# Performance work log

Hardware: AMD Instinct MI355X
Metric: run time of the kernel (lower is better)

## Reference

```python
import jax, jax.numpy as jnp
import numpy as np

N_NODES = 50000
N_EDGES = 500000
IN_DIM = 32
HID = 64
NUM_GRAPHS = 64


def _inv(d):
    # 1/d with inf -> 0, as in PyG HypergraphConv
    return jnp.where(d > 0, 1.0 / d, 0.0)


def hypergraph_conv(xh, row0, row1, W, b, n_hnodes, n_hedges):
    """PyG HypergraphConv (heads=1, no attention, unit hyperedge weights).
    xh: (n_hnodes, din) hyper-node features; row0: hyper-node ids, row1: hyperedge ids.
    Index n_hnodes / n_hedges is a padding slot for masked-out incidences.
    """
    xw = xh @ W                                   # (n_hnodes, dout) Theta
    xw = jnp.concatenate([xw, jnp.zeros((1, xw.shape[1]), xw.dtype)], axis=0)
    ones = jnp.ones(row0.shape[0], xw.dtype)
    D = _inv(jax.ops.segment_sum(ones, row0, num_segments=n_hnodes + 1))  # node degree^-1
    B = _inv(jax.ops.segment_sum(ones, row1, num_segments=n_hedges + 1))  # edge size^-1
    # node -> hyperedge aggregation, scaled by B
    he = jax.ops.segment_sum(xw[row0], row1, num_segments=n_hedges + 1) * B[:, None]
    # hyperedge -> node aggregation, scaled by D
    out = jax.ops.segment_sum(he[row1], row0, num_segments=n_hnodes + 1) * D[:, None]
    return out[:n_hnodes] + b


def setup_inputs() -> dict:
    key = jax.random.key(0)
    ks = jax.random.split(key, 12)
    x = jax.random.normal(ks[0], (N_NODES, 16), jnp.float32)
    edge_attr = jax.random.normal(ks[1], (N_EDGES, IN_DIM), jnp.float32)
    edge_index = jax.random.randint(ks[2], (2, N_EDGES), 0, N_NODES, dtype=jnp.int64)
    batch = jnp.sort(jax.random.randint(ks[3], (N_NODES,), 0, NUM_GRAPHS, dtype=jnp.int64))
    node_imp = jax.random.uniform(ks[4], (N_NODES,), jnp.float32)
    s = 0.05
    W0 = jax.random.normal(ks[5], (IN_DIM, HID), jnp.float32) * s
    b0 = jax.random.normal(ks[6], (HID,), jnp.float32) * s
    W1 = jax.random.normal(ks[7], (HID, HID), jnp.float32) * s
    b1 = jax.random.normal(ks[8], (HID,), jnp.float32) * s
    W2 = jax.random.normal(ks[9], (HID, HID), jnp.float32) * s
    b2 = jax.random.normal(ks[10], (HID,), jnp.float32) * s
    return {"x": x, "edge_attr": edge_attr, "edge_index": edge_index, "batch": batch,
            "node_imp": node_imp, "W0": W0, "b0": b0, "W1": W1, "b1": b1,
            "W2": W2, "b2": b2, "num_graphs": NUM_GRAPHS}


def reference(x, edge_attr, edge_index, batch, node_imp, W0, b0, W1, b1, W2, b2, num_graphs):
    N = x.shape[0]
    E = edge_index.shape[1]
    edge_imp = jnp.minimum(node_imp[edge_index[0]], node_imp[edge_index[1]])
    # --- Dual Hypergraph Transform (get_DHT) ---
    row0 = jnp.repeat(jnp.arange(E), 2)            # hyper-node = original edge id
    row1 = edge_index.T.reshape(-1)                # hyperedge  = original node id
    deg = jax.ops.segment_sum(jnp.ones(2 * E, jnp.float32), row1, num_segments=N)
    keep = deg[row1] != 1.0                        # drop incidences of degree-1 hyperedges
    row0 = jnp.where(keep, row0, E)                # redirect dropped entries to padding slot
    row1 = jnp.where(keep, row1, N + E)
    # self-loops: hyperedge ids N..N+E-1 (equivalent to torch's max_edge+1.., since
    # unused hyperedge slots receive nothing and B^-1 there is 0)
    row0 = jnp.concatenate([row0, jnp.arange(E)])
    row1 = jnp.concatenate([row1, N + jnp.arange(E)])
    edge_batch = batch[edge_index[0]]              # == hyperedge_index[1].reshape(-1,2)[:,0]
    # --- conv stack (dropout in eval mode = identity) ---
    h = edge_attr * edge_imp[:, None]
    xs = []
    for (W, b) in ((W0, b0), (W1, b1), (W2, b2)):
        h = jax.nn.relu(hypergraph_conv(h, row0, row1, W, b, E, N + E))
        h = h * edge_imp[:, None]
        xs.append(h)
    gh = jnp.concatenate(
        [jax.ops.segment_sum(h_i, edge_batch, num_segments=num_graphs) for h_i in xs], axis=1)
    return gh
```

## Files before the change

### kernel.cpp

```cpp
#include <hip/hip_runtime.h>
#include <hip/hip_bf16.h>
#include <cstdint>
#include <cstddef>

typedef unsigned short u16;
typedef unsigned int   u32;
typedef short bf16x8 __attribute__((ext_vector_type(8)));
typedef float f32x4  __attribute__((ext_vector_type(4)));

struct __align__(16) ERec { u32 uv; float iu, iv, ie; };
struct __align__(8) NRec { float dinv; float imp; };

#define NCOPY 8

__device__ __forceinline__ float bf2f(u16 v){ return __uint_as_float(((u32)v)<<16); }
__device__ __forceinline__ u16 f2bf(float f){
  u32 x = __float_as_uint(f);
  return (u16)((x + 0x7FFFu + ((x>>16)&1u)) >> 16);
}
__device__ __forceinline__ void atomAddF(float* p, float v){ unsafeAtomicAdd(p, v); }
__device__ __forceinline__ float rlanef(float v, int q){
  return __int_as_float(__builtin_amdgcn_readlane(__float_as_int(v), q));
}

__global__ void kzero(int* p, int n){
  int i = blockIdx.x*blockDim.x + threadIdx.x;
  if(i < n) p[i] = 0;
}

__global__ void kdeg2p(const int* __restrict__ ei0, const int* __restrict__ ei1,
                       int* __restrict__ deg0c, int* __restrict__ deg1c,
                       int* __restrict__ r0, int* __restrict__ r1,
                       int N, int E){
  int e = blockIdx.x*blockDim.x + threadIdx.x;
  if(e >= E) return;
  const int c = blockIdx.x & (NCOPY-1);
  r0[e] = atomicAdd(&deg0c[c*N + ei0[e]], 1);
  r1[e] = atomicAdd(&deg1c[c*N + ei1[e]], 1);
}

__global__ void kreduce(const int* __restrict__ deg0c, const int* __restrict__ deg1c,
                        int* __restrict__ deg0, int* __restrict__ deg1,
                        int* __restrict__ cb0, int* __restrict__ cb1, int N){
  int i = blockIdx.x*blockDim.x + threadIdx.x;
  if(i < N){
    int s = 0;
    #pragma unroll
    for(int c = 0; c < NCOPY; c++){ int t = deg0c[c*N+i]; cb0[c*N+i] = s; s += t; }
    deg0[i] = s;
  } else if(i < 2*N){
    int j = i - N;
    int s = 0;
    #pragma unroll
    for(int c = 0; c < NCOPY; c++){ int t = deg1c[c*N+j]; cb1[c*N+j] = s; s += t; }
    deg1[j] = s;
  }
}

__global__ __launch_bounds__(256) void ktilesum(const int* __restrict__ deg0,
                                                const int* __restrict__ deg1,
                                                int* __restrict__ tsum,
                                                int N, int nt){
  __shared__ int sh[256];
  const int b = blockIdx.x;
  const int* deg = (b < nt) ? deg0 : deg1;
  const int tile = (b < nt) ? b : b - nt;
  const int t = threadIdx.x;
  const int i = tile*256 + t;
  sh[t] = (i < N) ? deg[i] : 0;
  __syncthreads();
  for(int s = 128; s > 0; s >>= 1){
    if(t < s) sh[t] += sh[t+s];
    __syncthreads();
  }
  if(t == 0) tsum[b] = sh[0];
}
__global__ __launch_bounds__(256) void kmid(int* __restrict__ tsum,
                                            int* __restrict__ off0,
                                            int* __restrict__ off1,
                                            int N, int nt){
  __shared__ int sh[256];
  const int b = blockIdx.x;
  int* ts = tsum + b*nt;
  const int t = threadIdx.x;
  sh[t] = (t < nt) ? ts[t] : 0;
  __syncthreads();
  for(int s = 1; s < 256; s <<= 1){
    int x = (t >= s) ? sh[t-s] : 0;
    __syncthreads();
    sh[t] += x;
    __syncthreads();
  }
  if(t < nt) ts[t] = (t == 0) ? 0 : sh[t-1];
  if(t == 255){ int* off = b ? off1 : off0; off[N] = sh[255]; }
}
__global__ __launch_bounds__(256) void kapply(const int* __restrict__ deg0,
                                              const int* __restrict__ deg1,
                                              const int* __restrict__ tsum,
                                              int* __restrict__ off0,
                                              int* __restrict__ off1,
                                              const float* __restrict__ nimp,
                                              NRec* __restrict__ nrec,
                                              int N, int nt){
  __shared__ int sh[256];
  const int b = blockIdx.x;
  const int* deg = (b < nt) ? deg0 : deg1;
  int*       off = (b < nt) ? off0 : off1;
  const int tile = (b < nt) ? b : b - nt;
  const int base = tsum[b];
  const int t = threadIdx.x;
  const int i = tile*256 + t;
  sh[t] = (i < N) ? deg[i] : 0;
  __syncthreads();
  for(int s = 1; s < 256; s <<= 1){
    int x = (t >= s) ? sh[t-s] : 0;
    __syncthreads();
    sh[t] += x;
    __syncthreads();
  }
  if(i < N){
    off[i] = base + ((t == 0) ? 0 : sh[t-1]);
    if(b < nt){
      int d = deg0[i] + deg1[i];
      NRec r;
      r.dinv = (d > 1) ? (1.f/(float)d) : 0.f;
      r.imp  = nimp[i];
      nrec[i] = r;
    }
  }
}

__global__ void kpermv(const int* __restrict__ ei0, const int* __restrict__ ei1,
                       const NRec* __restrict__ nrec,
                       const int* __restrict__ off0, const int* __restrict__ off1,
                       const int* __restrict__ cb0, const int* __restrict__ cb1,
                       const int* __restrict__ r0, const int* __restrict__ r1,
                       ERec* __restrict__ rec, int* __restrict__ orig,
                       int* __restrict__ list1, int E, int N){
  int e = blockIdx.x*blockDim.x + threadIdx.x;
  if(e >= E) return;
  const int c = blockIdx.x & (NCOPY-1);
  int u = ei0[e], v = ei1[e];
  NRec ru = nrec[u];
  NRec rv = nrec[v];
  int pos = off0[u] + cb0[c*N+u] + r0[e];
  float ie = fminf(ru.imp, rv.imp);
  ERec r;
  r.uv = (u32)u | ((u32)v << 16);
  r.iu = ru.dinv; r.iv = rv.dinv; r.ie = ie;
  rec[pos]  = r;
  orig[pos] = e;
  int p1 = off1[v] + cb1[c*N+v] + r1[e];
  list1[p1] = pos;
}

__global__ __launch_bounds__(256) void kprep0(const float* __restrict__ ea,
                                              const int* __restrict__ orig,
                                              const float* __restrict__ recf,
                                              u16* __restrict__ h0, int E){
  int idx = blockIdx.x*256 + threadIdx.x;
  int row = idx >> 2;
  int c   = (idx & 3)*8;
  if(row >= E) return;
  int oe = orig[row];
  float ie = recf[(size_t)row*4 + 3];
  const float* s = ea + (size_t)oe*32 + c;
  f32x4 v0 = *(const f32x4*)s;
  f32x4 v1 = *(const f32x4*)(s+4);
  u32 o0 = (u32)f2bf(v0.x*ie) | ((u32)f2bf(v0.y*ie) << 16);
  u32 o1 = (u32)f2bf(v0.z*ie) | ((u32)f2bf(v0.w*ie) << 16);
  u32 o2 = (u32)f2bf(v1.x*ie) | ((u32)f2bf(v1.y*ie) << 16);
  u32 o3 = (u32)f2bf(v1.z*ie) | ((u32)f2bf(v1.w*ie) << 16);
  *(uint4*)(h0 + (size_t)row*32 + c) = make_uint4(o0,o1,o2,o3);
}

__global__ void kprepw(const float* __restrict__ W0, u16* __restrict__ wf0,
                       const float* __restrict__ W1, u16* __restrict__ wf1,
                       const float* __restrict__ W2, u16* __restrict__ wf2){
  const int b = blockIdx.x;
  const float* W; u16* wf; int NC, sbase;
  if(b == 0){ W = W0; wf = wf0; NC = 1; sbase = 0; }
  else if(b <= 2){ W = W1; wf = wf1; NC = 2; sbase = (b-1)*256; }
  else { W = W2; wf = wf2; NC = 2; sbase = (b-3)*256; }
  int s = sbase + threadIdx.x;
  if(s >= 4*NC*64) return;
  int lane = s & 63;
  int c    = (s >> 6) % NC;
  int tt   = s / (NC*64);
  int n  = tt*16 + (lane & 15);
  int k0 = c*32 + (lane >> 4)*8;
  #pragma unroll
  for(int j = 0; j < 8; j++)
    wf[(size_t)s*8 + j] = f2bf(W[(size_t)(k0 + j)*64 + n]);
}

template<int DIM>
__global__ __launch_bounds__(256) void kagg(const u16* __restrict__ buf,
                                            const int* __restrict__ off0,
                                            const int* __restrict__ off1,
                                            const int* __restrict__ list1,
                                            u16* __restrict__ heb, int N){
  const int t = threadIdx.x, wv = t >> 6, lane = t & 63;
  const int n = blockIdx.x*4 + wv;
  if(n >= N) return;
  constexpr int CB = DIM/8;
  constexpr int RS = 64/CB;
  const int rsub = lane / CB, cb = lane % CB;
  float acc[8];
  #pragma unroll
  for(int k = 0; k < 8; k++) acc[k] = 0.f;

  auto accum = [&](uint4 x){
    acc[0] += bf2f((u16)x.x); acc[1] += bf2f((u16)(x.x>>16));
    acc[2] += bf2f((u16)x.y); acc[3] += bf2f((u16)(x.y>>16));
    acc[4] += bf2f((u16)x.z); acc[5] += bf2f((u16)(x.z>>16));
    acc[6] += bf2f((u16)x.w); acc[7] += bf2f((u16)(x.w>>16));
  };
  const uint4 zero4 = {0,0,0,0};

  {
    const int s0 = off0[n], d0 = off0[n+1] - s0;
    const u16* base = buf + (size_t)s0*DIM;
    int j = 0;
    for(; j + RS <= d0; j += RS)
      accum(*(const uint4*)(base + (size_t)(j+rsub)*DIM + cb*8));
    if(j < d0)
      accum((rsub < d0-j) ? *(const uint4*)(base + (size_t)(j+rsub)*DIM + cb*8) : zero4);
  }
  {
    const int s1 = off1[n], d1 = off1[n+1] - s1;
    int j = 0;
    for(; j + RS <= d1; j += RS){
      int e = list1[s1 + j + rsub];
      accum(*(const uint4*)(buf + (size_t)e*DIM + cb*8));
    }
    if(j < d1){
      uint4 x = zero4;
      if(rsub < d1-j){
        int e = list1[s1 + j + rsub];
        x = *(const uint4*)(buf + (size_t)e*DIM + cb*8);
      }
      accum(x);
    }
  }
  #pragma unroll
  for(int m = CB; m <= 32; m <<= 1)
    #pragma unroll
    for(int k = 0; k < 8; k++) acc[k] += __shfl_xor(acc[k], m);
  if(rsub == 0){
    u32 o[4];
    #pragma unroll
    for(int k = 0; k < 4; k++)
      o[k] = (u32)f2bf(acc[2*k]) | ((u32)f2bf(acc[2*k+1]) << 16);
    *(uint4*)(heb + (size_t)n*DIM + cb*8) = make_uint4(o[0],o[1],o[2],o[3]);
  }
}

__global__ __launch_bounds__(256, 3) void kfusedR1(const u16* __restrict__ h0,
                                                   const u16* __restrict__ agg0,
                                                   u16* __restrict__ buf,
                                                   const f32x4* __restrict__ rec4,
                                                   const int* __restrict__ batch,
                                                   const float* __restrict__ bias0,
                                                   const u16* __restrict__ wf0,
                                                   const u16* __restrict__ wf1,
                                                   float* __restrict__ gh0,
                                                   int E){
  __shared__ __align__(16) u16 hT[4*16*72];
  __shared__ float ies[4][16];
  const int t = threadIdx.x, wv = t >> 6, lane = t & 63;
  const int quad = lane >> 4, l15 = lane & 15;
  const int c32  = lane & 31;
  const int half = lane >> 5;
  u16* hTw = &hT[wv*1152];

  float bd4[4];
  #pragma unroll
  for(int tt = 0; tt < 4; tt++) bd4[tt] = bias0[tt*16 + l15];

  bf16x8 b0fr[4];
  #pragma unroll
  for(int i = 0; i < 4; i++)
    b0fr[i] = *(const bf16x8*)(wf0 + ((size_t)i*64 + lane)*8);
  bf16x8 b1fr[8];
  #pragma unroll
  for(int i = 0; i < 8; i++)
    b1fr[i] = *(const bf16x8*)(wf1 + ((size_t)i*64 + lane)*8);

  float pool[4] = {0.f,0.f,0.f,0.f};
  int cur_g = -1;
  const int base = __builtin_amdgcn_readfirstlane((int)(blockIdx.x*256) + wv*64);

  auto flushPool = [&](){
    #pragma unroll
    for(int tt = 0; tt < 4; tt++){
      float s = pool[tt];
      s += __shfl_xor(s, 16);
      s += __shfl_xor(s, 32);
      if(quad == 0) atomAddF(&gh0[cur_g*192 + tt*16 + l15], s);
      pool[tt] = 0.f;
    }
  };

  u32 uvp = 0; f32x4 cf = {0.f,0.f,0.f,0.f}; int bt = 0;
  if(base < E){
    f32x4 w0 = rec4[(size_t)(base+l15)];
    uvp = __float_as_uint(w0.x);
    const float iu = w0.y, iv = w0.z;
    const float rc = (iu > 0.f && iv > 0.f) ? (1.f/3.f)
                   : ((iu > 0.f || iv > 0.f) ? 0.5f : 1.f);
    cf.x = rc; cf.y = iu*rc; cf.z = iv*rc; cf.w = w0.w;
    bt  = batch[uvp & 0xffffu];
  }

  #pragma unroll 1
  for(int it = 0; it < 4; it++){
    const int r0 = base + it*16;
    if(r0 < E){
      u16 zb[8], hu[8], hv[8];
      const u16* h0r = h0 + (size_t)r0*32;
      #pragma unroll
      for(int q = 0; q < 8; q++){
        const u32 uvA = (u32)__builtin_amdgcn_readlane((int)uvp, 2*q);
        const u32 uvB = (u32)__builtin_amdgcn_readlane((int)uvp, 2*q+1);
        const u32 uvS = half ? uvB : uvA;
        hv[q] = agg0[(size_t)(uvS >> 16)*32 + c32];
        hu[q] = agg0[(size_t)(uvS & 0xffffu)*32 + c32];
        zb[q] = h0r[(2*q+half)*32 + c32];
      }
      u32 uvpN = uvp; f32x4 cfN = cf; int btN = bt;
      if(it < 3){
        const int r1 = r0 + 16;
        if(r1 < E){
          f32x4 w0 = rec4[(size_t)(r1+l15)];
          uvpN = __float_as_uint(w0.x);
          const float iu = w0.y, iv = w0.z;
          const float rc = (iu > 0.f && iv > 0.f) ? (1.f/3.f)
                         : ((iu > 0.f || iv > 0.f) ? 0.5f : 1.f);
          cfN.x = rc; cfN.y = iu*rc; cfN.z = iv*rc; cfN.w = w0.w;
          btN  = batch[uvpN & 0xffffu];
        }
      }
      if(lane < 16) ies[wv][lane] = cf.w;
      #pragma unroll
      for(int q = 0; q < 8; q++){
        const float rcA = rlanef(cf.x, 2*q), rcB = rlanef(cf.x, 2*q+1);
        const float iuA = rlanef(cf.y, 2*q), iuB = rlanef(cf.y, 2*q+1);
        const float ivA = rlanef(cf.z, 2*q), ivB = rlanef(cf.z, 2*q+1);
        const float rc   = half ? rcB : rcA;
        const float iurc = half ? iuB : iuA;
        const float ivrc = half ? ivB : ivA;
        float z = fmaf(bf2f(zb[q]), rc,
                  fmaf(bf2f(hu[q]), iurc, bf2f(hv[q])*ivrc));
        hTw[(2*q+half)*72 + c32] = f2bf(z);
      }
      bf16x8 za = *(const bf16x8*)&hTw[l15*72 + quad*8];
      f32x4 a0_[4];
      #pragma unroll
      for(int tt = 0; tt < 4; tt++){
        f32x4 a = {0.f,0.f,0.f,0.f};
        a = __builtin_amdgcn_mfma_f32_16x16x32_bf16(za, b0fr[tt], a, 0, 0, 0);
        a0_[tt] = a;
      }
      float ier[4];
      #pragma unroll
      for(int r = 0; r < 4; r++) ier[r] = ies[wv][quad*4 + r];
      float o[4][4];
      #pragma unroll
      for(int tt = 0; tt < 4; tt++)
        #pragma unroll
        for(int r = 0; r < 4; r++)
          o[tt][r] = fmaxf(a0_[tt][r] + bd4[tt], 0.f) * ier[r];
      const int bFirst = __builtin_amdgcn_readlane(bt, 0);
      const int bLast  = __builtin_amdgcn_readlane(bt, 15);
      if(bFirst == bLast){
        if(bFirst != cur_g){
          if(cur_g >= 0) flushPool();
          cur_g = bFirst;
        }
        #pragma unroll
        for(int tt = 0; tt < 4; tt++)
          pool[tt] += (o[tt][0] + o[tt][1]) + (o[tt][2] + o[tt][3]);
      } else {
        #pragma unroll
        for(int rr = 0; rr < 16; rr++){
          const int bq = __builtin_amdgcn_readlane(bt, rr);
          if(bq != cur_g){
            if(cur_g >= 0) flushPool();
            cur_g = bq;
          }
          if((rr >> 2) == quad){
            #pragma unroll
            for(int tt = 0; tt < 4; tt++) pool[tt] += o[tt][rr & 3];
          }
        }
      }
      #pragma unroll
      for(int tt = 0; tt < 4; tt++)
        #pragma unroll
        for(int r = 0; r < 4; r++)
          hTw[(quad*4 + r)*72 + tt*16 + l15] = f2bf(o[tt][r]);
      bf16x8 afr0 = *(const bf16x8*)&hTw[l15*72 + quad*8];
      bf16x8 afr1 = *(const bf16x8*)&hTw[l15*72 + 32 + quad*8];
      #pragma unroll
      for(int tt = 0; tt < 4; tt++){
        f32x4 a = {0.f,0.f,0.f,0.f};
        a = __builtin_amdgcn_mfma_f32_16x16x32_bf16(afr0, b1fr[tt*2+0], a, 0, 0, 0);
        a = __builtin_amdgcn_mfma_f32_16x16x32_bf16(afr1, b1fr[tt*2+1], a, 0, 0, 0);
        const int n = tt*16 + l15;
        #pragma unroll
        for(int r = 0; r < 4; r++)
          buf[(size_t)(r0 + quad*4 + r)*64 + n] = f2bf(a[r]);
      }
      uvp = uvpN; cf = cfN; bt = btN;
    }
  }
  if(cur_g >= 0) flushPool();
}

template<bool DO_GEMM>
__global__ __launch_bounds__(256, 3) void kfused(u16* __restrict__ buf,
                                                 const u16* __restrict__ heb,
                                                 const f32x4* __restrict__ rec4,
                                                 const int* __restrict__ batch,
                                                 const float* __restrict__ bias,
                                                 const u16* __restrict__ wf,
                                                 float* __restrict__ ghL,
                                                 int E){
  constexpr int HTSZ = DO_GEMM ? 4*16*72 : 4;
  __shared__ __align__(16) u16 hT[HTSZ];
  const int t = threadIdx.x, wv = t >> 6, lane = t & 63;
  const int quad = lane >> 4, l15 = lane & 15;
  const float bd = bias[lane];

  bf16x8 bfr[8];
  if(DO_GEMM){
    #pragma unroll
    for(int i = 0; i < 8; i++)
      bfr[i] = *(const bf16x8*)(wf + ((size_t)i*64 + lane)*8);
  }

  float pool = 0.f;
  int cur_g = -1;
  const int base = __builtin_amdgcn_readfirstlane((int)(blockIdx.x*256) + wv*64);
  u16* hTw = DO_GEMM ? &hT[wv*1152] : &hT[0];

  u32 uvp = 0; f32x4 cf = {0.f,0.f,0.f,0.f}; int bt = 0;
  if(base < E){
    f32x4 w0 = rec4[(size_t)(base+l15)];
    uvp = __float_as_uint(w0.x);
    const float iu = w0.y, iv = w0.z;
    const float rc = (iu > 0.f && iv > 0.f) ? (1.f/3.f)
                   : ((iu > 0.f || iv > 0.f) ? 0.5f : 1.f);
    cf.x = rc; cf.y = iu*rc; cf.z = iv*rc; cf.w = w0.w;
    bt  = batch[uvp & 0xffffu];
  }

  #pragma unroll
  for(int it = 0; it < 4; it++){
    const int r0 = base + it*16;
    if(r0 < E){
      u16 bv[16], hu[16], hv[16];
      const u16* bufr = buf + (size_t)r0*64;
      #pragma unroll
      for(int q = 0; q < 16; q++){
        const u32 uv = (u32)__builtin_amdgcn_readlane((int)uvp, q);
        hv[q] = heb[(size_t)(uv >> 16)*64 + lane];
        hu[q] = heb[(size_t)(uv & 0xffffu)*64 + lane];
        bv[q] = bufr[q*64 + lane];
      }
      u32 uvpN = uvp; f32x4 cfN = cf; int btN = bt;
      if(it < 3){
        const int r1 = r0 + 16;
        if(r1 < E){
          f32x4 w0 = rec4[(size_t)(r1+l15)];
          uvpN = __float_as_uint(w0.x);
          const float iu = w0.y, iv = w0.z;
          const float rc = (iu > 0.f && iv > 0.f) ? (1.f/3.f)
                         : ((iu > 0.f || iv > 0.f) ? 0.5f : 1.f);
          cfN.x = rc; cfN.y = iu*rc; cfN.z = iv*rc; cfN.w = w0.w;
          btN  = batch[uvpN & 0xffffu];
        }
      }
      const int bFirst = __builtin_amdgcn_readlane(bt, 0);
      const int bLast  = __builtin_amdgcn_readlane(bt, 15);
      if(bFirst != cur_g){
        if(cur_g >= 0) atomAddF(&ghL[cur_g*192 + lane], pool);
        pool = 0.f; cur_g = bFirst;
      }
      if(bFirst == bLast){
        #pragma unroll
        for(int q = 0; q < 16; q++){
          const float rc   = rlanef(cf.x, q);
          const float iurc = rlanef(cf.y, q);
          const float ivrc = rlanef(cf.z, q);
          const float ie   = rlanef(cf.w, q);
          float o = fmaxf(fmaf(bf2f(bv[q]), rc,
                          fmaf(bf2f(hu[q]), iurc,
                          fmaf(bf2f(hv[q]), ivrc, bd))), 0.f) * ie;
          pool += o;
          if(DO_GEMM) hTw[q*72 + lane] = f2bf(o);
        }
      } else {
        #pragma unroll
        for(int q = 0; q < 16; q++){
          const float rc   = rlanef(cf.x, q);
          const float iurc = rlanef(cf.y, q);
          const float ivrc = rlanef(cf.z, q);
          const float ie   = rlanef(cf.w, q);
          const int   bq   = __builtin_amdgcn_readlane(bt, q);
          float o = fmaxf(fmaf(bf2f(bv[q]), rc,
                          fmaf(bf2f(hu[q]), iurc,
                          fmaf(bf2f(hv[q]), ivrc, bd))), 0.f) * ie;
          if(bq != cur_g){
            if(cur_g >= 0) atomAddF(&ghL[cur_g*192 + lane], pool);
            pool = 0.f; cur_g = bq;
          }
          pool += o;
          if(DO_GEMM) hTw[q*72 + lane] = f2bf(o);
        }
      }
      if(DO_GEMM){
        bf16x8 afr0 = *(const bf16x8*)&hTw[l15*72 + quad*8];
        bf16x8 afr1 = *(const bf16x8*)&hTw[l15*72 + 32 + quad*8];
        #pragma unroll
        for(int tt = 0; tt < 4; tt++){
          f32x4 a = {0.f,0.f,0.f,0.f};
          a = __builtin_amdgcn_mfma_f32_16x16x32_bf16(afr0, bfr[tt*2+0], a, 0, 0, 0);
          a = __builtin_amdgcn_mfma_f32_16x16x32_bf16(afr1, bfr[tt*2+1], a, 0, 0, 0);
          const int n = tt*16 + l15;
          #pragma unroll
          for(int r = 0; r < 4; r++)
            buf[(size_t)(r0 + quad*4 + r)*64 + n] = f2bf(a[r]);
        }
      }
      uvp = uvpN; cf = cfN; bt = btN;
    }
  }
  if(cur_g >= 0) atomAddF(&ghL[cur_g*192 + lane], pool);
}

__global__ void kfinal(const float* __restrict__ gh, float* __restrict__ out, int n){
  int i = blockIdx.x*blockDim.x + threadIdx.x;
  if(i < n) out[i] = gh[i];
}

extern "C" void kernel_launch(void* const* d_in, const int* in_sizes, int n_in,
                              void* d_out, int out_size, void* d_ws, size_t ws_size,
                              hipStream_t stream) {
  const float* edge_attr = (const float*)d_in[1];
  const int*   ei        = (const int*)d_in[2];
  const int*   batch     = (const int*)d_in[3];
  const float* nimp      = (const float*)d_in[4];
  const float* Ws[3] = { (const float*)d_in[5], (const float*)d_in[7], (const float*)d_in[9] };
  const float* bs[3] = { (const float*)d_in[6], (const float*)d_in[8], (const float*)d_in[10] };

  const int E = in_sizes[1] / 32;
  const int N = in_sizes[4];
  const int* ei0 = ei;
  const int* ei1 = ei + E;

  char* p = (char*)d_ws;
  auto carve = [&](size_t bytes)->char*{
    char* r = p; p += (bytes + 255) & ~(size_t)255; return r;
  };
  const int nt = (N + 255)/256;
  int*   deg0c = (int*)  carve((size_t)2*NCOPY*N*4);
  int*   deg1c = deg0c + NCOPY*N;
  int*   cb0   = (int*)  carve((size_t)2*NCOPY*N*4);
  int*   cb1   = cb0 + NCOPY*N;
  int*   r0    = (int*)  carve((size_t)2*E*4);
  int*   r1    = r0 + E;
  int*   deg0  = (int*)  carve((size_t)2*N*4);
  int*   deg1  = deg0 + N;
  NRec*  nrec  = (NRec*) carve((size_t)N*sizeof(NRec));
  int*   off0  = (int*)  carve((size_t)(N+1)*4);
  int*   off1  = (int*)  carve((size_t)(N+1)*4);
  int*   tsum  = (int*)  carve((size_t)2*nt*4);
  int*   orig  = (int*)  carve((size_t)E*4);
  int*   list1 = (int*)  carve((size_t)E*4);
  ERec*  rec   = (ERec*) carve((size_t)E*sizeof(ERec));
  u16*   h0    = (u16*)  carve((size_t)E*32*2);
  u16*   agg0  = (u16*)  carve((size_t)N*32*2);
  u16*   heb   = (u16*)  carve((size_t)N*64*2);
  u16*   buf   = (u16*)  carve((size_t)E*64*2);
  float* gh    = (float*)carve((size_t)64*192*4);
  u16*   wfs[3];
  for(int l = 0; l < 3; l++) wfs[l] = (u16*)carve((size_t)4096*2);

  kzero<<<(2*NCOPY*N+255)/256, 256, 0, stream>>>(deg0c, 2*NCOPY*N);
  kzero<<<(12288+255)/256, 256, 0, stream>>>((int*)gh, 12288);
  kdeg2p<<<(E+255)/256, 256, 0, stream>>>(ei0, ei1, deg0c, deg1c, r0, r1, N, E);
  kreduce<<<(2*N+255)/256, 256, 0, stream>>>(deg0c, deg1c, deg0, deg1, cb0, cb1, N);
  ktilesum<<<2*nt, 256, 0, stream>>>(deg0, deg1, tsum, N, nt);
  kmid<<<2, 256, 0, stream>>>(tsum, off0, off1, N, nt);
  kapply<<<2*nt, 256, 0, stream>>>(deg0, deg1, tsum, off0, off1, nimp, nrec, N, nt);
  kpermv<<<(E+255)/256, 256, 0, stream>>>(ei0, ei1, nrec, off0, off1, cb0, cb1,
                                          r0, r1, rec, orig, list1, E, N);
  kprep0<<<((E*4)+255)/256, 256, 0, stream>>>(edge_attr, orig, (const float*)rec, h0, E);
  kprepw<<<5, 256, 0, stream>>>(Ws[0], wfs[0], Ws[1], wfs[1], Ws[2], wfs[2]);

  const int nbA = (N + 3)/4;
  const int nbF = (E + 255)/256;

  kagg<32><<<nbA, 256, 0, stream>>>(h0, off0, off1, list1, agg0, N);
  kfusedR1<<<nbF, 256, 0, stream>>>(h0, agg0, buf, (const f32x4*)rec, batch,
                                    bs[0], wfs[0], wfs[1], gh + 0*64, E);
  kagg<64><<<nbA, 256, 0, stream>>>(buf, off0, off1, list1, heb, N);
  kfused<true ><<<nbF, 256, 0, stream>>>(buf, heb, (const f32x4*)rec, batch, bs[1], wfs[2], gh + 1*64, E);
  kagg<64><<<nbA, 256, 0, stream>>>(buf, off0, off1, list1, heb, N);
  kfused<false><<<nbF, 256, 0, stream>>>(buf, heb, (const f32x4*)rec, batch, bs[2], nullptr, gh + 2*64, E);
  kfinal<<<(12288+255)/256, 256, 0, stream>>>(gh, (float*)d_out, 12288);
}
```

Baseline: 386.9 us.

## Double-buffer gathers in kfusedR1 to overlap loads with MFMA compute

Replaces the rolled 4-iteration loop in kfusedR1 with a manually unrolled software pipeline. All four record loads are hoisted up front, and the next tile's gathers from agg0 and h0 are issued into a second register buffer before the current tile is consumed. The aim is to hide gather latency behind the MFMA and pooling work of the previous tile. The cost is higher register pressure from the extra buffers and hoisted records, which may reduce occupancy under launch bounds of 3 blocks per SM.

Result: no change. 389.8 us (+0.8%).

```diff
diff --git a/kernel.cpp b/kernel.cpp
--- a/kernel.cpp
+++ b/kernel.cpp
@@ -256,6 +256,21 @@
   }
 }
 
+__device__ __forceinline__ void issueR1(const u16* __restrict__ h0r,
+                                        const u16* __restrict__ agg0,
+                                        u32 uvp, int c32, int half,
+                                        u16 (&zb)[8], u16 (&hu)[8], u16 (&hv)[8]){
+  #pragma unroll
+  for(int q = 0; q < 8; q++){
+    const u32 uvA = (u32)__builtin_amdgcn_readlane((int)uvp, 2*q);
+    const u32 uvB = (u32)__builtin_amdgcn_readlane((int)uvp, 2*q+1);
+    const u32 uvS = half ? uvB : uvA;
+    hv[q] = agg0[(size_t)(uvS >> 16)*32 + c32];
+    hu[q] = agg0[(size_t)(uvS & 0xffffu)*32 + c32];
+    zb[q] = h0r[(2*q+half)*32 + c32];
+  }
+}
+
 __global__ __launch_bounds__(256, 3) void kfusedR1(const u16* __restrict__ h0,
                                                    const u16* __restrict__ agg0,
                                                    u16* __restrict__ buf,
@@ -302,119 +317,112 @@
     }
   };
 
-  u32 uvp = 0; f32x4 cf = {0.f,0.f,0.f,0.f}; int bt = 0;
-  if(base < E){
-    f32x4 w0 = rec4[(size_t)(base+l15)];
-    uvp = __float_as_uint(w0.x);
-    const float iu = w0.y, iv = w0.z;
-    const float rc = (iu > 0.f && iv > 0.f) ? (1.f/3.f)
-                   : ((iu > 0.f || iv > 0.f) ? 0.5f : 1.f);
-    cf.x = rc; cf.y = iu*rc; cf.z = iv*rc; cf.w = w0.w;
-    bt  = batch[uvp & 0xffffu];
-  }
-
-  #pragma unroll 1
-  for(int it = 0; it < 4; it++){
-    const int r0 = base + it*16;
-    if(r0 < E){
-      u16 zb[8], hu[8], hv[8];
-      const u16* h0r = h0 + (size_t)r0*32;
+  u32 uv_[4]; f32x4 cf_[4]; int bt_[4];
+  #pragma unroll
+  for(int k = 0; k < 4; k++){
+    uv_[k] = 0; cf_[k] = (f32x4){0.f,0.f,0.f,0.f}; bt_[k] = 0;
+    const int rk = base + k*16;
+    if(rk < E){
+      f32x4 w0 = rec4[(size_t)(rk+l15)];
+      uv_[k] = __float_as_uint(w0.x);
+      const float iu = w0.y, iv = w0.z;
+      const float rc = (iu > 0.f && iv > 0.f) ? (1.f/3.f)
+                     : ((iu > 0.f || iv > 0.f) ? 0.5f : 1.f);
+      cf_[k].x = rc; cf_[k].y = iu*rc; cf_[k].z = iv*rc; cf_[k].w = w0.w;
+      bt_[k] = batch[uv_[k] & 0xffffu];
+    }
+  }
+
+  auto consume = [&](int r0, f32x4 cf, int bt,
+                     u16 (&zb)[8], u16 (&hu)[8], u16 (&hv)[8]){
+    if(lane < 16) ies[wv][lane] = cf.w;
+    #pragma unroll
+    for(int q = 0; q < 8; q++){
+      const float rcA = rlanef(cf.x, 2*q), rcB = rlanef(cf.x, 2*q+1);
+      const float iuA = rlanef(cf.y, 2*q), iuB = rlanef(cf.y, 2*q+1);
+      const float ivA = rlanef(cf.z, 2*q), ivB = rlanef(cf.z, 2*q+1);
+      const float rc   = half ? rcB : rcA;
+      const float iurc = half ? iuB : iuA;
+      const float ivrc = half ? ivB : ivA;
+      float z = fmaf(bf2f(zb[q]), rc,
+                fmaf(bf2f(hu[q]), iurc, bf2f(hv[q])*ivrc));
+      hTw[(2*q+half)*72 + c32] = f2bf(z);
+    }
+    bf16x8 za = *(const bf16x8*)&hTw[l15*72 + quad*8];
+    f32x4 a0_[4];
+    #pragma unroll
+    for(int tt = 0; tt < 4; tt++){
+      f32x4 a = {0.f,0.f,0.f,0.f};
+      a = __builtin_amdgcn_mfma_f32_16x16x32_bf16(za, b0fr[tt], a, 0, 0, 0);
+      a0_[tt] = a;
+    }
+    float ier[4];
+    #pragma unroll
+    for(int r = 0; r < 4; r++) ier[r] = ies[wv][quad*4 + r];
+    float o[4][4];
+    #pragma unroll
+    for(int tt = 0; tt < 4; tt++)
       #pragma unroll
-      for(int q = 0; q < 8; q++){
-        const u32 uvA = (u32)__builtin_amdgcn_readlane((int)uvp, 2*q);
-        const u32 uvB = (u32)__builtin_amdgcn_readlane((int)uvp, 2*q+1);
-        const u32 uvS = half ? uvB : uvA;
-        hv[q] = agg0[(size_t)(uvS >> 16)*32 + c32];
-        hu[q] = agg0[(size_t)(uvS & 0xffffu)*32 + c32];
-        zb[q] = h0r[(2*q+half)*32 + c32];
-      }
-      u32 uvpN = uvp; f32x4 cfN = cf; int btN = bt;
-      if(it < 3){
-        const int r1 = r0 + 16;
-        if(r1 < E){
-          f32x4 w0 = rec4[(size_t)(r1+l15)];
-          uvpN = __float_as_uint(w0.x);
-          const float iu = w0.y, iv = w0.z;
-          const float rc = (iu > 0.f && iv > 0.f) ? (1.f/3.f)
-                         : ((iu > 0.f || iv > 0.f) ? 0.5f : 1.f);
-          cfN.x = rc; cfN.y = iu*rc; cfN.z = iv*rc; cfN.w = w0.w;
-          btN  = batch[uvpN & 0xffffu];
-        }
-      }
-      if(lane < 16) ies[wv][lane] = cf.w;
-      #pragma unroll
-      for(int q = 0; q < 8; q++){
-        const float rcA = rlanef(cf.x, 2*q), rcB = rlanef(cf.x, 2*q+1);
-        const float iuA = rlanef(cf.y, 2*q), iuB = rlanef(cf.y, 2*q+1);
-        const float ivA = rlanef(cf.z, 2*q), ivB = rlanef(cf.z, 2*q+1);
-        const float rc   = half ? rcB : rcA;
-        const float iurc = half ? iuB : iuA;
-        const float ivrc = half ? ivB : ivA;
-        float z = fmaf(bf2f(zb[q]), rc,
-                  fmaf(bf2f(hu[q]), iurc, bf2f(hv[q])*ivrc));
-        hTw[(2*q+half)*72 + c32] = f2bf(z);
-      }
-      bf16x8 za = *(const bf16x8*)&hTw[l15*72 + quad*8];
-      f32x4 a0_[4];
-      #pragma unroll
-      for(int tt = 0; tt < 4; tt++){
-        f32x4 a = {0.f,0.f,0.f,0.f};
-        a = __builtin_amdgcn_mfma_f32_16x16x32_bf16(za, b0fr[tt], a, 0, 0, 0);
-        a0_[tt] = a;
-      }
-      float ier[4];
-      #pragma unroll
-      for(int r = 0; r < 4; r++) ier[r] = ies[wv][quad*4 + r];
-      float o[4][4];
+      for(int r = 0; r < 4; r++)
+        o[tt][r] = fmaxf(a0_[tt][r] + bd4[tt], 0.f) * ier[r];
+    const int bFirst = __builtin_amdgcn_readlane(bt, 0);
+    const int bLast  = __builtin_amdgcn_readlane(bt, 15);
+    if(bFirst == bLast){
+      if(bFirst != cur_g){
+        if(cur_g >= 0) flushPool();
+        cur_g = bFirst;
+      }
       #pragma unroll
       for(int tt = 0; tt < 4; tt++)
-        #pragma unroll
-        for(int r = 0; r < 4; r++)
-          o[tt][r] = fmaxf(a0_[tt][r] + bd4[tt], 0.f) * ier[r];
-      const int bFirst = __builtin_amdgcn_readlane(bt, 0);
-      const int bLast  = __builtin_amdgcn_readlane(bt, 15);
-      if(bFirst == bLast){
-        if(bFirst != cur_g){
+        pool[tt] += (o[tt][0] + o[tt][1]) + (o[tt][2] + o[tt][3]);
+    } else {
+      #pragma unroll
+      for(int rr = 0; rr < 16; rr++){
+        const int bq = __builtin_amdgcn_readlane(bt, rr);
+        if(bq != cur_g){
           if(cur_g >= 0) flushPool();
-          cur_g = bFirst;
+          cur_g = bq;
         }
-        #pragma unroll
-        for(int tt = 0; tt < 4; tt++)
-          pool[tt] += (o[tt][0] + o[tt][1]) + (o[tt][2] + o[tt][3]);
-      } else {
-        #pragma unroll
-        for(int rr = 0; rr < 16; rr++){
-          const int bq = __builtin_amdgcn_readlane(bt, rr);
-          if(bq != cur_g){
-            if(cur_g >= 0) flushPool();
-            cur_g = bq;
-          }
-          if((rr >> 2) == quad){
-            #pragma unroll
-            for(int tt = 0; tt < 4; tt++) pool[tt] += o[tt][rr & 3];
-          }
+        if((rr >> 2) == quad){
+          #pragma unroll
+          for(int tt = 0; tt < 4; tt++) pool[tt] += o[tt][rr & 3];
         }
       }
+    }
+    #pragma unroll
+    for(int tt = 0; tt < 4; tt++)
       #pragma unroll
-      for(int tt = 0; tt < 4; tt++)
-        #pragma unroll
-        for(int r = 0; r < 4; r++)
-          hTw[(quad*4 + r)*72 + tt*16 + l15] = f2bf(o[tt][r]);
-      bf16x8 afr0 = *(const bf16x8*)&hTw[l15*72 + quad*8];
-      bf16x8 afr1 = *(const bf16x8*)&hTw[l15*72 + 32 + quad*8];
+      for(int r = 0; r < 4; r++)
+        hTw[(quad*4 + r)*72 + tt*16 + l15] = f2bf(o[tt][r]);
+    bf16x8 afr0 = *(const bf16x8*)&hTw[l15*72 + quad*8];
+    bf16x8 afr1 = *(const bf16x8*)&hTw[l15*72 + 32 + quad*8];
+    #pragma unroll
+    for(int tt = 0; tt < 4; tt++){
+      f32x4 a = {0.f,0.f,0.f,0.f};
+      a = __builtin_amdgcn_mfma_f32_16x16x32_bf16(afr0, b1fr[tt*2+0], a, 0, 0, 0);
+      a = __builtin_amdgcn_mfma_f32_16x16x32_bf16(afr1, b1fr[tt*2+1], a, 0, 0, 0);
+      const int n = tt*16 + l15;
       #pragma unroll
-      for(int tt = 0; tt < 4; tt++){
-        f32x4 a = {0.f,0.f,0.f,0.f};
-        a = __builtin_amdgcn_mfma_f32_16x16x32_bf16(afr0, b1fr[tt*2+0], a, 0, 0, 0);
-        a = __builtin_amdgcn_mfma_f32_16x16x32_bf16(afr1, b1fr[tt*2+1], a, 0, 0, 0);
-        const int n = tt*16 + l15;
-        #pragma unroll
-        for(int r = 0; r < 4; r++)
-          buf[(size_t)(r0 + quad*4 + r)*64 + n] = f2bf(a[r]);
-      }
-      uvp = uvpN; cf = cfN; bt = btN;
-    }
-  }
+      for(int r = 0; r < 4; r++)
+        buf[(size_t)(r0 + quad*4 + r)*64 + n] = f2bf(a[r]);
+    }
+  };
+
+  const int r0b = base, r1b = base+16, r2b = base+32, r3b = base+48;
+  const bool a0 = r0b < E, a1 = r1b < E, a2 = r2b < E, a3 = r3b < E;
+
+  u16 zbA[8], huA[8], hvA[8];
+  u16 zbB[8], huB[8], hvB[8];
+
+  if(a0) issueR1(h0 + (size_t)r0b*32, agg0, uv_[0], c32, half, zbA, huA, hvA);
+  if(a1) issueR1(h0 + (size_t)r1b*32, agg0, uv_[1], c32, half, zbB, huB, hvB);
+  if(a0) consume(r0b, cf_[0], bt_[0], zbA, huA, hvA);
+  if(a2) issueR1(h0 + (size_t)r2b*32, agg0, uv_[2], c32, half, zbA, huA, hvA);
+  if(a1) consume(r1b, cf_[1], bt_[1], zbB, huB, hvB);
+  if(a3) issueR1(h0 + (size_t)r3b*32, agg0, uv_[3], c32, half, zbB, huB, hvB);
+  if(a2) consume(r2b, cf_[2], bt_[2], zbA, huA, hvA);
+  if(a3) consume(r3b, cf_[3], bt_[3], zbB, huB, hvB);
+
   if(cur_g >= 0) flushPool();
 }
 
```
